# Optimization experiments

Measured on AMD Instinct MI355X. Metric: run time of the kernel, lower is better.

Reference implementation:

```python
import jax, jax.numpy as jnp
import numpy as np

N_NODES = 100000
N_EDGES = 1600000


def spmm(edge_row, edge_col, edge_w, h):
    # out[r] = sum_{e: row[e]=r} w[e] * h[col[e]]   (sparse adj @ dense h)
    msgs = h[edge_col] * edge_w[:, None]  # [E, F]
    return jax.ops.segment_sum(msgs, edge_row, num_segments=N_NODES)


def setup_inputs() -> dict:
    key = jax.random.key(0)
    ks = jax.random.split(key, 6)
    x = jax.random.normal(ks[0], (N_NODES, 256), dtype=jnp.float32)
    edge_row = jax.random.randint(ks[1], (N_EDGES,), 0, N_NODES, dtype=jnp.int32)
    edge_col = jax.random.randint(ks[2], (N_EDGES,), 0, N_NODES, dtype=jnp.int32)
    edge_w = jax.random.uniform(ks[3], (N_EDGES,), dtype=jnp.float32)
    W1 = jax.random.normal(ks[4], (256, 128), dtype=jnp.float32) * (1.0 / np.sqrt(256))
    b1 = jnp.zeros((128,), dtype=jnp.float32)
    W2 = jax.random.normal(ks[5], (128, 40), dtype=jnp.float32) * (1.0 / np.sqrt(128))
    b2 = jnp.zeros((40,), dtype=jnp.float32)
    return {"x": x, "edge_row": edge_row, "edge_col": edge_col, "edge_w": edge_w,
            "W1": W1, "b1": b1, "W2": W2, "b2": b2}


def reference(x, edge_row, edge_col, edge_w, W1, b1, W2, b2):
    # eval-mode GCN forward (dropout inactive, no BN)
    h = spmm(edge_row, edge_col, edge_w, x @ W1) + b1  # [N, hidden]
    h = jax.nn.relu(h)
    out = spmm(edge_row, edge_col, edge_w, h @ W2) + b2  # [N, classes]
    return jax.nn.log_softmax(out, axis=1)
```

## Files before the change

kernel.cpp:

```cpp
#include <hip/hip_runtime.h>
#include <math.h>

#define F1 256
#define F2 128
#define F3 40
#define H2S 64
#define RPB 256
#define RSH 8
#define TPB 8192

typedef unsigned short ushort_t;
typedef __attribute__((ext_vector_type(8))) short bf16x8;
typedef __attribute__((ext_vector_type(4))) float f32x4;

__device__ inline ushort_t f2bf(float f) {
  unsigned u = __builtin_bit_cast(unsigned, f);
  u += 0x7FFF + ((u >> 16) & 1);
  return (ushort_t)(u >> 16);
}
__device__ inline float bf2f(ushort_t b) {
  unsigned u = ((unsigned)b) << 16;
  return __builtin_bit_cast(float, u);
}
__device__ inline float i2f(int b) { return __builtin_bit_cast(float, b); }


__global__ __launch_bounds__(256) void k_cnt(const int* __restrict__ row, int* __restrict__ cnt,
                                             int E, int G, int NBIN) {
  __shared__ int h[400];
  int tid = threadIdx.x, blk = blockIdx.x;
  for (int i = tid; i < NBIN; i += 256) h[i] = 0;
  __syncthreads();
  int base = blk * TPB, lim = min(base + TPB, E);
  for (int i = base + tid; i < lim; i += 256) atomicAdd(&h[row[i] >> RSH], 1);
  __syncthreads();
  for (int i = tid; i < NBIN; i += 256) cnt[i * G + blk] = h[i];
}

__global__ __launch_bounds__(256) void k_scan1(const int* __restrict__ in, int* __restrict__ out,
                                               int* __restrict__ aux, int n) {
  __shared__ int lds[256];
  int tid = threadIdx.x;
  int base = blockIdx.x * 1024 + tid * 4;
  int v0 = 0, v1 = 0, v2 = 0, v3 = 0;
  if (base + 0 < n) v0 = in[base + 0];
  if (base + 1 < n) v1 = in[base + 1];
  if (base + 2 < n) v2 = in[base + 2];
  if (base + 3 < n) v3 = in[base + 3];
  int s = v0 + v1 + v2 + v3;
  lds[tid] = s;
  __syncthreads();
  for (int off = 1; off < 256; off <<= 1) {
    int t = (tid >= off) ? lds[tid - off] : 0;
    __syncthreads();
    lds[tid] += t;
    __syncthreads();
  }
  int excl = (tid > 0) ? lds[tid - 1] : 0;
  if (tid == 255) aux[blockIdx.x] = lds[255];
  if (base + 0 < n) out[base + 0] = excl;
  if (base + 1 < n) out[base + 1] = excl + v0;
  if (base + 2 < n) out[base + 2] = excl + v0 + v1;
  if (base + 3 < n) out[base + 3] = excl + v0 + v1 + v2;
}

__global__ __launch_bounds__(128) void k_scan_aux(int* __restrict__ aux, int nb) {
  __shared__ int lds[128];
  int tid = threadIdx.x;
  int v = (tid < nb) ? aux[tid] : 0;
  lds[tid] = v;
  __syncthreads();
  for (int off = 1; off < 128; off <<= 1) {
    int t = (tid >= off) ? lds[tid - off] : 0;
    __syncthreads();
    lds[tid] += t;
    __syncthreads();
  }
  int excl = (tid > 0) ? lds[tid - 1] : 0;
  if (tid < nb) aux[tid] = excl;
}

__global__ __launch_bounds__(256) void k_scan_add(int* __restrict__ out, const int* __restrict__ aux,
                                                  int n, int E) {
  int add = aux[blockIdx.x];
  int base = blockIdx.x * 1024 + threadIdx.x * 4;
#pragma unroll
  for (int i = 0; i < 4; i++)
    if (base + i < n) out[base + i] += add;
  if (blockIdx.x == 0 && threadIdx.x == 0) out[n] = E;
}

__global__ __launch_bounds__(256) void k_scatter1(const int* __restrict__ row, const int* __restrict__ col,
                                                  const float* __restrict__ w, const int* __restrict__ cntoff,
                                                  int2* __restrict__ epk2, int E, int G, int NBIN) {
  __shared__ int cur[400];
  int tid = threadIdx.x, blk = blockIdx.x;
  for (int i = tid; i < NBIN; i += 256) cur[i] = cntoff[i * G + blk];
  __syncthreads();
  int base = blk * TPB, lim = min(base + TPB, E);
  for (int i = base + tid; i < lim; i += 256) {
    int r = row[i];
    int pos = atomicAdd(&cur[r >> RSH], 1);
    epk2[pos] = make_int2(((r & (RPB - 1)) << 17) | col[i], __builtin_bit_cast(int, w[i]));
  }
}

__global__ __launch_bounds__(256) void k_binsort(const int* __restrict__ cntoff, const int2* __restrict__ epk2,
                                                 int* __restrict__ ip, int2* __restrict__ epk,
                                                 int G, int NBIN, int N, int E) {
  __shared__ int sc[256], cur[256];
  int tid = threadIdx.x, b = blockIdx.x;
  int s = cntoff[b * G], eend = cntoff[(b + 1) * G];
  cur[tid] = 0;
  __syncthreads();
  for (int i = s + tid; i < eend; i += 256) atomicAdd(&cur[epk2[i].x >> 17], 1);
  __syncthreads();
  int d = cur[tid];
  sc[tid] = d;
  __syncthreads();
  for (int o = 1; o < 256; o <<= 1) {
    int t = (tid >= o) ? sc[tid - o] : 0;
    __syncthreads();
    sc[tid] += t;
    __syncthreads();
  }
  int excl = (tid > 0) ? sc[tid - 1] : 0;
  __syncthreads();
  cur[tid] = excl;
  int gr = (b << RSH) + tid;
  if (gr <= N) ip[gr] = s + excl;
  if (b == 0 && tid == 0) ip[N] = E;
  __syncthreads();
  for (int i = s + tid; i < eend; i += 256) {
    int2 rec = epk2[i];
    int local = rec.x >> 17, c = rec.x & 0x1FFFF;
    int p = s + atomicAdd(&cur[local], 1);
    epk[p] = make_int2(c, rec.y);
  }
}

__global__ __launch_bounds__(256) void k_w1prep(const float* __restrict__ W1, ushort_t* __restrict__ w1p) {
  int t = blockIdx.x * 256 + threadIdx.x;
  if (t < 8 * 128 * 40) {
    int kk = t % 40;
    int rem = t / 40;
    int c = rem & 127;
    int kt = rem >> 7;
    w1p[t] = (kk < 32) ? f2bf(W1[(size_t)(kt * 32 + kk) * F2 + c]) : (ushort_t)0;
  }
}

__global__ __launch_bounds__(256) void k_w2prep(const float* __restrict__ W2, ushort_t* __restrict__ w2p) {
  int idx = blockIdx.x * 256 + threadIdx.x;
  if (idx < 4 * 3 * 64 * 8) {
    int j = idx & 7;
    int rem = idx >> 3;
    int l = rem & 63;
    int g = rem >> 6;
    int t = g % 3, kt = g / 3;
    int colc = t * 16 + (l & 15);
    int k = kt * 32 + (l >> 4) * 8 + j;
    w2p[idx] = (colc < F3) ? f2bf(W2[(size_t)k * F3 + colc]) : (ushort_t)0;
  }
}

#define XPAD 264
__global__ __launch_bounds__(256) void k_gemm1(const float* __restrict__ x, const ushort_t* __restrict__ w1p,
                                               ushort_t* __restrict__ h0bf, int N) {
  __shared__ ushort_t xs[64 * XPAD];
  __shared__ ushort_t wb[2][128 * 40];
  const int tid = threadIdx.x;
  const int lane = tid & 63;
  const int w = tid >> 6;
  const int r0 = blockIdx.x * 64;

#pragma unroll 4
  for (int i = 0; i < 16; ++i) {
    int row = w * 16 + i;
    int gr = r0 + row;
    if (gr >= N) gr = 0;
    float4 v = ((const float4*)(x + (size_t)gr * F1))[lane];
    ushort_t* d = &xs[row * XPAD + lane * 4];
    d[0] = f2bf(v.x); d[1] = f2bf(v.y); d[2] = f2bf(v.z); d[3] = f2bf(v.w);
  }
  {
    const uint4* src = (const uint4*)w1p;
    uint4* dst = (uint4*)&wb[0][0];
    for (int o = tid; o < 640; o += 256) dst[o] = src[o];
  }
  __syncthreads();

  f32x4 acc[8];
#pragma unroll
  for (int t = 0; t < 8; ++t) acc[t] = (f32x4){0.f, 0.f, 0.f, 0.f};

  const int arow = w * 16 + (lane & 15);
  const int kg = (lane >> 4) * 8;

  for (int kt = 0; kt < 8; ++kt) {
    if (kt < 7) {
      const uint4* src = (const uint4*)(w1p + (size_t)(kt + 1) * 128 * 40);
      uint4* dst = (uint4*)&wb[(kt + 1) & 1][0];
      for (int o = tid; o < 640; o += 256) dst[o] = src[o];
    }
    bf16x8 a = *(const bf16x8*)&xs[arow * XPAD + kt * 32 + kg];
    const ushort_t* wbb = &wb[kt & 1][0];
#pragma unroll
    for (int t = 0; t < 8; ++t) {
      bf16x8 bfr = *(const bf16x8*)&wbb[(t * 16 + (lane & 15)) * 40 + kg];
      acc[t] = __builtin_amdgcn_mfma_f32_16x16x32_bf16(a, bfr, acc[t], 0, 0, 0);
    }
    __syncthreads();
  }

#pragma unroll
  for (int t = 0; t < 8; ++t) {
    int gc = t * 16 + (lane & 15);
#pragma unroll
    for (int j = 0; j < 4; ++j) {
      int gr = r0 + w * 16 + (lane >> 4) * 4 + j;
      if (gr < N) h0bf[(size_t)gr * F2 + gc] = f2bf(acc[t][j]);
    }
  }
}

__global__ __launch_bounds__(256) void k_spmm1(const int* __restrict__ ip, const int2* __restrict__ epk,
                                               const ushort_t* __restrict__ h0bf,
                                               const float* __restrict__ b1, ushort_t* __restrict__ hbf) {
  int node = blockIdx.x * 4 + (threadIdx.x >> 6);
  int lane = threadIdx.x & 63;
  int e0 = __builtin_amdgcn_readfirstlane(ip[node]);
  int e1 = __builtin_amdgcn_readfirstlane(ip[node + 1]);
  float ax0 = 0.f, ay0 = 0.f, ax1 = 0.f, ay1 = 0.f;
  float ax2 = 0.f, ay2 = 0.f, ax3 = 0.f, ay3 = 0.f;
  int e = e0;
  for (; e + 4 <= e1; e += 4) {
    int2 p0 = epk[e], p1 = epk[e + 1], p2 = epk[e + 2], p3 = epk[e + 3];
    ushort2 v0 = *(const ushort2*)(h0bf + (size_t)p0.x * F2 + lane * 2);
    ushort2 v1 = *(const ushort2*)(h0bf + (size_t)p1.x * F2 + lane * 2);
    ushort2 v2 = *(const ushort2*)(h0bf + (size_t)p2.x * F2 + lane * 2);
    ushort2 v3 = *(const ushort2*)(h0bf + (size_t)p3.x * F2 + lane * 2);
    float w0 = i2f(p0.y), w1 = i2f(p1.y), w2 = i2f(p2.y), w3 = i2f(p3.y);
    ax0 = fmaf(w0, bf2f(v0.x), ax0); ay0 = fmaf(w0, bf2f(v0.y), ay0);
    ax1 = fmaf(w1, bf2f(v1.x), ax1); ay1 = fmaf(w1, bf2f(v1.y), ay1);
    ax2 = fmaf(w2, bf2f(v2.x), ax2); ay2 = fmaf(w2, bf2f(v2.y), ay2);
    ax3 = fmaf(w3, bf2f(v3.x), ax3); ay3 = fmaf(w3, bf2f(v3.y), ay3);
  }
  for (; e < e1; ++e) {
    int2 p = epk[e];
    ushort2 v = *(const ushort2*)(h0bf + (size_t)p.x * F2 + lane * 2);
    float wt = i2f(p.y);
    ax0 = fmaf(wt, bf2f(v.x), ax0); ay0 = fmaf(wt, bf2f(v.y), ay0);
  }
  float ax = (ax0 + ax1) + (ax2 + ax3);
  float ay = (ay0 + ay1) + (ay2 + ay3);
  float2 bb = *(const float2*)(b1 + lane * 2);
  ushort2 r;
  r.x = f2bf(fmaxf(ax + bb.x, 0.f));
  r.y = f2bf(fmaxf(ay + bb.y, 0.f));
  *(ushort2*)(hbf + (size_t)node * F2 + lane * 2) = r;
}

__global__ __launch_bounds__(256) void k_gemm2(const ushort_t* __restrict__ hbf, const ushort_t* __restrict__ w2p,
                                               ushort_t* __restrict__ h2p, int N) {
  const int tid = threadIdx.x;
  const int lane = tid & 63;
  const int w = tid >> 6;
  const int r0 = blockIdx.x * 64;
  const int arow = r0 + w * 16 + (lane & 15);
  const int ar = (arow < N) ? arow : 0;
  const int kg = (lane >> 4) * 8;

  bf16x8 a[4];
#pragma unroll
  for (int kt = 0; kt < 4; ++kt)
    a[kt] = *(const bf16x8*)(hbf + (size_t)ar * F2 + kt * 32 + kg);

  f32x4 acc[3];
#pragma unroll
  for (int t = 0; t < 3; ++t) acc[t] = (f32x4){0.f, 0.f, 0.f, 0.f};

#pragma unroll
  for (int kt = 0; kt < 4; ++kt) {
#pragma unroll
    for (int t = 0; t < 3; ++t) {
      bf16x8 b = *(const bf16x8*)(w2p + (size_t)(((kt * 3 + t) * 64) + lane) * 8);
      acc[t] = __builtin_amdgcn_mfma_f32_16x16x32_bf16(a[kt], b, acc[t], 0, 0, 0);
    }
  }

#pragma unroll
  for (int t = 0; t < 3; ++t) {
    int gc = t * 16 + (lane & 15);
    if (gc < F3) {
#pragma unroll
      for (int j = 0; j < 4; ++j) {
        int gr = r0 + w * 16 + (lane >> 4) * 4 + j;
        if (gr < N) h2p[(size_t)gr * H2S + gc] = f2bf(acc[t][j]);
      }
    }
  }
  for (int idx = tid; idx < 64 * 24; idx += 256) {
    int row = idx / 24, pc = F3 + idx % 24;
    int gr = r0 + row;
    if (gr < N) h2p[(size_t)gr * H2S + pc] = 0;
  }
}

__global__ __launch_bounds__(256) void k_spmm2lsm(const int* __restrict__ ip, const int2* __restrict__ epk,
                                                  const ushort_t* __restrict__ h2p,
                                                  const float* __restrict__ b2, float* __restrict__ out) {
  int node = blockIdx.x * 4 + (threadIdx.x >> 6);
  int lane = threadIdx.x & 63;
  int e0 = __builtin_amdgcn_readfirstlane(ip[node]);
  int e1 = __builtin_amdgcn_readfirstlane(ip[node + 1]);
  float a0 = 0.f, a1 = 0.f, a2 = 0.f, a3 = 0.f;
  int e = e0;
  for (; e + 4 <= e1; e += 4) {
    int2 p0 = epk[e], p1 = epk[e + 1], p2 = epk[e + 2], p3 = epk[e + 3];
    float v0 = bf2f(h2p[(size_t)p0.x * H2S + lane]);
    float v1 = bf2f(h2p[(size_t)p1.x * H2S + lane]);
    float v2 = bf2f(h2p[(size_t)p2.x * H2S + lane]);
    float v3 = bf2f(h2p[(size_t)p3.x * H2S + lane]);
    a0 = fmaf(i2f(p0.y), v0, a0);
    a1 = fmaf(i2f(p1.y), v1, a1);
    a2 = fmaf(i2f(p2.y), v2, a2);
    a3 = fmaf(i2f(p3.y), v3, a3);
  }
  for (; e < e1; ++e) {
    int2 p = epk[e];
    float v = bf2f(h2p[(size_t)p.x * H2S + lane]);
    a0 = fmaf(i2f(p.y), v, a0);
  }
  float acc = (a0 + a1) + (a2 + a3);
  float logit = (lane < F3) ? (acc + b2[lane]) : -INFINITY;
  float m = logit;
#pragma unroll
  for (int off = 32; off > 0; off >>= 1) m = fmaxf(m, __shfl_xor(m, off));
  float ex = (lane < F3) ? __expf(logit - m) : 0.f;
  float s = ex;
#pragma unroll
  for (int off = 32; off > 0; off >>= 1) s += __shfl_xor(s, off);
  if (lane < F3) out[(size_t)node * F3 + lane] = logit - m - __logf(s);
}

extern "C" void kernel_launch(void* const* d_in, const int* in_sizes, int n_in,
                              void* d_out, int out_size, void* d_ws, size_t ws_size,
                              hipStream_t stream) {
  const float* x     = (const float*)d_in[0];
  const int* erow    = (const int*)d_in[1];
  const int* ecol_in = (const int*)d_in[2];
  const float* ew_in = (const float*)d_in[3];
  const float* W1    = (const float*)d_in[4];
  const float* b1    = (const float*)d_in[5];
  const float* W2    = (const float*)d_in[6];
  const float* b2    = (const float*)d_in[7];
  float* out = (float*)d_out;

  const int N = in_sizes[0] / F1;
  const int E = in_sizes[1];

  const int G = (E + TPB - 1) / TPB;
  const int NBIN = (N + RPB - 1) >> RSH;
  const int M = NBIN * G;
  const int nb2 = (M + 1023) / 1024;

  ushort_t* h0bf = (ushort_t*)d_ws;
  int2* epk2 = (int2*)d_ws;
  ushort_t* h2p = h0bf;
  ushort_t* hbf = h0bf + (size_t)N * F2;
  int* ip = (int*)(hbf + (size_t)N * F2);
  int* cnt = ip + (N + 32);
  int* cntoff = cnt + M + 8;
  int* aux = cntoff + M + 64;
  int2* epk = (int2*)(aux + 128);
  ushort_t* w1p = (ushort_t*)(epk + E);
  ushort_t* w2p = w1p + 40960;

  hipLaunchKernelGGL(k_cnt, dim3(G), dim3(256), 0, stream, erow, cnt, E, G, NBIN);
  hipLaunchKernelGGL(k_scan1, dim3(nb2), dim3(256), 0, stream, cnt, cntoff, aux, M);
  hipLaunchKernelGGL(k_scan_aux, dim3(1), dim3(128), 0, stream, aux, nb2);
  hipLaunchKernelGGL(k_scan_add, dim3(nb2), dim3(256), 0, stream, cntoff, aux, M, E);
  hipLaunchKernelGGL(k_scatter1, dim3(G), dim3(256), 0, stream, erow, ecol_in, ew_in, cntoff, epk2, E, G, NBIN);
  hipLaunchKernelGGL(k_binsort, dim3(NBIN), dim3(256), 0, stream, cntoff, epk2, ip, epk, G, NBIN, N, E);
  hipLaunchKernelGGL(k_w1prep, dim3((8 * 128 * 40 + 255) / 256), dim3(256), 0, stream, W1, w1p);
  hipLaunchKernelGGL(k_w2prep, dim3((4 * 3 * 64 * 8 + 255) / 256), dim3(256), 0, stream, W2, w2p);
  hipLaunchKernelGGL(k_gemm1, dim3((N + 63) / 64), dim3(256), 0, stream, x, w1p, h0bf, N);
  hipLaunchKernelGGL(k_spmm1, dim3(N / 4), dim3(256), 0, stream, ip, epk, h0bf, b1, hbf);
  hipLaunchKernelGGL(k_gemm2, dim3((N + 63) / 64), dim3(256), 0, stream, hbf, w2p, h2p, N);
  hipLaunchKernelGGL(k_spmm2lsm, dim3(N / 4), dim3(256), 0, stream, ip, epk, h2p, b2, out);
}
```

Before: 244.5 us.

## Drop LDS staging in gemm1; load x and fragment-packed W1 directly to registers

W1 is now pre-packed in MFMA B-fragment order, so each lane reads its bf16x8 operand straight from global memory (L2/L1-resident) instead of double-buffering W1 tiles through LDS. The x tile is also loaded per lane directly into A fragments with in-register bf16 conversion, which removes the shared-memory staging and all the __syncthreads. This frees LDS and should raise occupancy and remove barrier stalls. The cost is more global and cache traffic for W1, since each wave rereads the whole packed weight matrix, and x loads per lane are strided 32-byte pieces rather than fully coalesced rows.

```diff
diff --git a/kernel.cpp b/kernel.cpp
--- a/kernel.cpp
+++ b/kernel.cpp
@@ -139,14 +139,16 @@
   }
 }
 
-__global__ __launch_bounds__(256) void k_w1prep(const float* __restrict__ W1, ushort_t* __restrict__ w1p) {
-  int t = blockIdx.x * 256 + threadIdx.x;
-  if (t < 8 * 128 * 40) {
-    int kk = t % 40;
-    int rem = t / 40;
-    int c = rem & 127;
-    int kt = rem >> 7;
-    w1p[t] = (kk < 32) ? f2bf(W1[(size_t)(kt * 32 + kk) * F2 + c]) : (ushort_t)0;
+__global__ __launch_bounds__(256) void k_w1prep(const float* __restrict__ W1, ushort_t* __restrict__ w1pf) {
+  int idx = blockIdx.x * 256 + threadIdx.x;
+  if (idx < 8 * 8 * 64 * 8) {
+    int j = idx & 7;
+    int l = (idx >> 3) & 63;
+    int t = (idx >> 9) & 7;
+    int kt = idx >> 12;
+    int k = kt * 32 + (l >> 4) * 8 + j;
+    int c = t * 16 + (l & 15);
+    w1pf[idx] = f2bf(W1[(size_t)k * F2 + c]);
   }
 }
 
@@ -164,53 +166,35 @@
   }
 }
 
-#define XPAD 264
-__global__ __launch_bounds__(256) void k_gemm1(const float* __restrict__ x, const ushort_t* __restrict__ w1p,
+__global__ __launch_bounds__(256) void k_gemm1(const float* __restrict__ x, const ushort_t* __restrict__ w1pf,
                                                ushort_t* __restrict__ h0bf, int N) {
-  __shared__ ushort_t xs[64 * XPAD];
-  __shared__ ushort_t wb[2][128 * 40];
   const int tid = threadIdx.x;
   const int lane = tid & 63;
   const int w = tid >> 6;
   const int r0 = blockIdx.x * 64;
-
-#pragma unroll 4
-  for (int i = 0; i < 16; ++i) {
-    int row = w * 16 + i;
-    int gr = r0 + row;
-    if (gr >= N) gr = 0;
-    float4 v = ((const float4*)(x + (size_t)gr * F1))[lane];
-    ushort_t* d = &xs[row * XPAD + lane * 4];
-    d[0] = f2bf(v.x); d[1] = f2bf(v.y); d[2] = f2bf(v.z); d[3] = f2bf(v.w);
-  }
-  {
-    const uint4* src = (const uint4*)w1p;
-    uint4* dst = (uint4*)&wb[0][0];
-    for (int o = tid; o < 640; o += 256) dst[o] = src[o];
-  }
-  __syncthreads();
+  const int arow = r0 + w * 16 + (lane & 15);
+  const int ar = (arow < N) ? arow : 0;
+  const int kg = (lane >> 4) * 8;
+  const float* xr = x + (size_t)ar * F1 + kg;
 
   f32x4 acc[8];
 #pragma unroll
   for (int t = 0; t < 8; ++t) acc[t] = (f32x4){0.f, 0.f, 0.f, 0.f};
 
-  const int arow = w * 16 + (lane & 15);
-  const int kg = (lane >> 4) * 8;
-
+#pragma unroll
   for (int kt = 0; kt < 8; ++kt) {
-    if (kt < 7) {
-      const uint4* src = (const uint4*)(w1p + (size_t)(kt + 1) * 128 * 40);
-      uint4* dst = (uint4*)&wb[(kt + 1) & 1][0];
-      for (int o = tid; o < 640; o += 256) dst[o] = src[o];
+    float4 v0 = *(const float4*)(xr + kt * 32);
+    float4 v1 = *(const float4*)(xr + kt * 32 + 4);
+    bf16x8 a;
+    a[0] = (short)f2bf(v0.x); a[1] = (short)f2bf(v0.y);
+    a[2] = (short)f2bf(v0.z); a[3] = (short)f2bf(v0.w);
+    a[4] = (short)f2bf(v1.x); a[5] = (short)f2bf(v1.y);
+    a[6] = (short)f2bf(v1.z); a[7] = (short)f2bf(v1.w);
+#pragma unroll
+    for (int t = 0; t < 8; ++t) {
+      bf16x8 b = *(const bf16x8*)(w1pf + (size_t)(((kt * 8 + t) * 64) + lane) * 8);
+      acc[t] = __builtin_amdgcn_mfma_f32_16x16x32_bf16(a, b, acc[t], 0, 0, 0);
     }
-    bf16x8 a = *(const bf16x8*)&xs[arow * XPAD + kt * 32 + kg];
-    const ushort_t* wbb = &wb[kt & 1][0];
-#pragma unroll
-    for (int t = 0; t < 8; ++t) {
-      bf16x8 bfr = *(const bf16x8*)&wbb[(t * 16 + (lane & 15)) * 40 + kg];
-      acc[t] = __builtin_amdgcn_mfma_f32_16x16x32_bf16(a, bfr, acc[t], 0, 0, 0);
-    }
-    __syncthreads();
   }
 
 #pragma unroll
@@ -374,8 +358,8 @@
   int* cntoff = cnt + M + 8;
   int* aux = cntoff + M + 64;
   int2* epk = (int2*)(aux + 128);
-  ushort_t* w1p = (ushort_t*)(epk + E);
-  ushort_t* w2p = w1p + 40960;
+  ushort_t* w1pf = (ushort_t*)(epk + E);
+  ushort_t* w2p = w1pf + 32768;
 
   hipLaunchKernelGGL(k_cnt, dim3(G), dim3(256), 0, stream, erow, cnt, E, G, NBIN);
   hipLaunchKernelGGL(k_scan1, dim3(nb2), dim3(256), 0, stream, cnt, cntoff, aux, M);
@@ -383,9 +367,9 @@
   hipLaunchKernelGGL(k_scan_add, dim3(nb2), dim3(256), 0, stream, cntoff, aux, M, E);
   hipLaunchKernelGGL(k_scatter1, dim3(G), dim3(256), 0, stream, erow, ecol_in, ew_in, cntoff, epk2, E, G, NBIN);
   hipLaunchKernelGGL(k_binsort, dim3(NBIN), dim3(256), 0, stream, cntoff, epk2, ip, epk, G, NBIN, N, E);
-  hipLaunchKernelGGL(k_w1prep, dim3((8 * 128 * 40 + 255) / 256), dim3(256), 0, stream, W1, w1p);
+  hipLaunchKernelGGL(k_w1prep, dim3(128), dim3(256), 0, stream, W1, w1pf);
   hipLaunchKernelGGL(k_w2prep, dim3((4 * 3 * 64 * 8 + 255) / 256), dim3(256), 0, stream, W2, w2p);
-  hipLaunchKernelGGL(k_gemm1, dim3((N + 63) / 64), dim3(256), 0, stream, x, w1p, h0bf, N);
+  hipLaunchKernelGGL(k_gemm1, dim3((N + 63) / 64), dim3(256), 0, stream, x, w1pf, h0bf, N);
   hipLaunchKernelGGL(k_spmm1, dim3(N / 4), dim3(256), 0, stream, ip, epk, h0bf, b1, hbf);
   hipLaunchKernelGGL(k_gemm2, dim3((N + 63) / 64), dim3(256), 0, stream, hbf, w2p, h2p, N);
   hipLaunchKernelGGL(k_spmm2lsm, dim3(N / 4), dim3(256), 0, stream, ip, epk, h2p, b2, out);
```

Measured after the change: 223.6 us. -8.6%, faster.
